# Kernel optimization log

Hardware: AMD Instinct MI355X
Metric: run time of the kernel (lower is better)

## Reference

```python
import jax, jax.numpy as jnp
import numpy as np

N = 100000   # nodes
E = 1600000  # edges (avg degree 16)
D = 128      # in_channels == hidden_channels
H = 4        # heads
C = D // H   # per-head channels = 32


def leaky(x, slope):
    return jnp.where(x >= 0, x, slope * x)


def setup_inputs() -> dict:
    key = jax.random.key(0)
    ks = jax.random.split(key, 12)
    s = 1.0 / np.sqrt(D)
    return {
        "x": jax.random.normal(ks[0], (N, D), jnp.float32),
        "edge_index": jax.random.randint(ks[1], (2, E), 0, N, jnp.int32),
        "edge_type": jax.random.randint(ks[2], (E,), 0, 8, jnp.int32),
        # linear1 (first_layer=True): LeakyReLU(0.01) -> Linear(D, D)
        "W1": jax.random.normal(ks[3], (D, D), jnp.float32) * s,
        "b1": jnp.zeros((D,), jnp.float32),
        # GATConv params: lin (no bias), att_src/att_dst [1,H,C], output bias [H*C]
        "Wg": jax.random.normal(ks[4], (D, D), jnp.float32) * s,
        "att_src": jax.random.normal(ks[5], (1, H, C), jnp.float32) * s,
        "att_dst": jax.random.normal(ks[6], (1, H, C), jnp.float32) * s,
        "bias_g": jnp.zeros((D,), jnp.float32),
        # linear2: LeakyReLU(0.01) -> Linear(D, D)
        "W2": jax.random.normal(ks[7], (D, D), jnp.float32) * s,
        "b2": jnp.zeros((D,), jnp.float32),
    }


def reference(x, edge_index, edge_type, W1, b1, Wg, att_src, att_dst, bias_g, W2, b2):
    # dropout layers act in eval mode (identity); edge_type is unused by forward.
    # linear1: LeakyReLU(0.01) then Linear
    x = leaky(x, 0.01) @ W1.T + b1                      # [N, D]

    # GATConv (add_self_loops=False, concat heads)
    h = (x @ Wg.T).reshape(N, H, C)                     # [N, H, C]
    a_src = jnp.sum(h * att_src, axis=-1)               # [N, H]
    a_dst = jnp.sum(h * att_dst, axis=-1)               # [N, H]

    src, dst = edge_index[0], edge_index[1]
    alpha = leaky(a_src[src] + a_dst[dst], 0.2)          # [E, H]

    # segment softmax over destination nodes (numerically stable)
    amax = jax.ops.segment_max(alpha, dst, num_segments=N)   # [N, H], -inf for empty
    amax = jnp.where(jnp.isfinite(amax), amax, 0.0)
    ex = jnp.exp(alpha - amax[dst])                      # [E, H]
    denom = jax.ops.segment_sum(ex, dst, num_segments=N) # [N, H]
    coeff = ex / (denom[dst] + 1e-16)                    # [E, H]

    msg = h[src] * coeff[:, :, None]                     # [E, H, C]
    out = jax.ops.segment_sum(msg, dst, num_segments=N)  # [N, H, C]
    out = out.reshape(N, H * C) + bias_g                 # [N, D]

    # linear2: LeakyReLU(0.01) then Linear; Dropout(0.3) identity at eval
    out = leaky(out, 0.01) @ W2.T + b2                   # [N, D]
    return out
```

## Files before the change

kernel.cpp:

```cpp
#include <hip/hip_runtime.h>
#include <hip/hip_bf16.h>

#define D128 128

typedef __attribute__((ext_vector_type(8))) short bf16x8;
typedef __attribute__((ext_vector_type(4))) float f32x4;

__device__ __forceinline__ float b2f(unsigned short u) {
    union { unsigned int i; float f; } z;
    z.i = ((unsigned int)u) << 16;
    return z.f;
}

__device__ __forceinline__ unsigned short f2b(float f) {
    union { float f; unsigned int i; } z;
    z.f = f;
    unsigned int r = z.i + 0x7FFFu + ((z.i >> 16) & 1u);
    return (unsigned short)(r >> 16);
}

__device__ __forceinline__ f32x4 mfma16(bf16x8 a, bf16x8 b, f32x4 c) {
    return __builtin_amdgcn_mfma_f32_16x16x32_bf16(a, b, c, 0, 0, 0);
}

#define CHUNK 8192
#define MAXBINS 512
#define BINCAP 8192
#define XBB 1536

__global__ __launch_bounds__(256) void k_prep1(
    const float* __restrict__ x,
    const float* __restrict__ W1, const float* __restrict__ Wg,
    const float* __restrict__ b1,
    const int* __restrict__ ei, int* __restrict__ M,
    float* __restrict__ Wc, float* __restrict__ bc,
    unsigned short* __restrict__ xb,
    int N, int E, int B, int nbins)
{
    __shared__ float wgr[256];
    __shared__ int hist[MAXBINS];
    const int t = threadIdx.x;
    if (blockIdx.x < 64) {
        const int i0 = blockIdx.x * 2;
        wgr[t] = Wg[i0 * 128 + t];
        __syncthreads();
        const int half = t >> 7;
        const int j = t & 127;
        const float* wr = &wgr[half * 128];
        float acc = 0.f;
        #pragma unroll 4
        for (int k = 0; k < 128; ++k)
            acc += wr[k] * W1[k * 128 + j];
        Wc[(i0 + half) * 128 + j] = acc;
        if (j == 0) {
            float ab = 0.f;
            for (int k = 0; k < 128; ++k) ab += wr[k] * b1[k];
            bc[i0 + half] = ab;
        }
    } else if (blockIdx.x < 64 + B) {
        const int chunk = blockIdx.x - 64;
        for (int i = t; i < nbins; i += 256) hist[i] = 0;
        __syncthreads();
        const int base = chunk * CHUNK;
        const int end = min(base + CHUNK, E);
        for (int e = base + t; e < end; e += 256)
            atomicAdd(&hist[ei[E + e] >> 8], 1);
        __syncthreads();
        for (int i = t; i < nbins; i += 256)
            M[i * B + chunk] = hist[i];
    } else {
        const size_t total = (size_t)N * 128;
        const size_t stride = (size_t)XBB * 256 * 8;
        for (size_t i = ((size_t)(blockIdx.x - 64 - B) * 256 + t) * 8; i + 8 <= total; i += stride) {
            float4 f0 = *(const float4*)(x + i);
            float4 f1 = *(const float4*)(x + i + 4);
            float v[8] = { f0.x, f0.y, f0.z, f0.w, f1.x, f1.y, f1.z, f1.w };
            union { uint4 q; unsigned short s[8]; } o;
            #pragma unroll
            for (int jj = 0; jj < 8; ++jj) {
                float f = v[jj];
                f = f >= 0.f ? f : 0.01f * f;
                o.s[jj] = f2b(f);
            }
            *(uint4*)(xb + i) = o.q;
        }
    }
}

__global__ __launch_bounds__(256) void k_prep2s(
    const float* __restrict__ Wc, const float* __restrict__ bc,
    const float* __restrict__ att_s, const float* __restrict__ att_d,
    const float* __restrict__ W2,
    unsigned short* __restrict__ Wcat, unsigned short* __restrict__ W2l,
    float* __restrict__ lbias,
    const int* __restrict__ M, int* __restrict__ scanned,
    int* __restrict__ bsum, int nM)
{
    __shared__ int lds[256];
    const int b = blockIdx.x, t = threadIdx.x;
    if (b < 9) {
        const int q = b * 256 + t;
        const int ct = q >> 8, rem = q & 255;
        const int ks = rem >> 6, lane = rem & 63;
        const int ldiv = lane >> 4, lmod = lane & 15;
        const int kb = ks * 32 + ldiv * 8;
        float v[8];
        if (ct < 8) {
            const int rho = ct * 16 + lmod;
            const float4 a = *(const float4*)(Wc + rho * 128 + kb);
            const float4 bq = *(const float4*)(Wc + rho * 128 + kb + 4);
            v[0] = a.x; v[1] = a.y; v[2] = a.z; v[3] = a.w;
            v[4] = bq.x; v[5] = bq.y; v[6] = bq.z; v[7] = bq.w;
        } else {
            #pragma unroll
            for (int e = 0; e < 8; ++e) v[e] = 0.f;
            if (lmod < 8) {
                const int hh = lmod & 3;
                const float* av = lmod < 4 ? att_s : att_d;
                for (int c = 0; c < 32; ++c) {
                    const float w = av[hh * 32 + c];
                    const float* wrow = Wc + (hh * 32 + c) * 128 + kb;
                    #pragma unroll
                    for (int e = 0; e < 8; ++e) v[e] += w * wrow[e];
                }
            }
        }
        union { uint4 qq; unsigned short s[8]; } o;
        #pragma unroll
        for (int e = 0; e < 8; ++e) o.s[e] = f2b(v[e]);
        *(uint4*)(Wcat + q * 8) = o.qq;
    } else if (b < 17) {
        const int q = (b - 9) * 256 + t;
        const int ct = q >> 8, rem = q & 255;
        const int ks = rem >> 6, lane = rem & 63;
        const int ldiv = lane >> 4, lmod = lane & 15;
        const int kb = ks * 32 + ldiv * 8;
        const int rho = ct * 16 + lmod;
        const float4 a = *(const float4*)(W2 + rho * 128 + kb);
        const float4 bq = *(const float4*)(W2 + rho * 128 + kb + 4);
        union { uint4 qq; unsigned short s[8]; } o;
        o.s[0] = f2b(a.x); o.s[1] = f2b(a.y); o.s[2] = f2b(a.z); o.s[3] = f2b(a.w);
        o.s[4] = f2b(bq.x); o.s[5] = f2b(bq.y); o.s[6] = f2b(bq.z); o.s[7] = f2b(bq.w);
        *(uint4*)(W2l + q * 8) = o.qq;
    } else if (b == 17) {
        if (t < 144) {
            float v = 0.f;
            if (t < 128) v = bc[t];
            else if (t < 136) {
                const int hh = (t - 128) & 3;
                const float* av = t < 132 ? att_s : att_d;
                for (int c = 0; c < 32; ++c) v += av[hh * 32 + c] * bc[hh * 32 + c];
            }
            lbias[t] = v;
        }
    } else {
        const int sid = b - 18;
        const int g0 = sid * 1024 + t * 4;
        int v0 = g0     < nM ? M[g0]     : 0;
        int v1 = g0 + 1 < nM ? M[g0 + 1] : 0;
        int v2 = g0 + 2 < nM ? M[g0 + 2] : 0;
        int v3 = g0 + 3 < nM ? M[g0 + 3] : 0;
        const int s = v0 + v1 + v2 + v3;
        lds[t] = s;
        __syncthreads();
        #pragma unroll
        for (int off = 1; off < 256; off <<= 1) {
            int tv = t >= off ? lds[t - off] : 0;
            __syncthreads();
            lds[t] += tv;
            __syncthreads();
        }
        int run = lds[t] - s;
        if (g0     < nM) scanned[g0]     = run;
        run += v0;
        if (g0 + 1 < nM) scanned[g0 + 1] = run;
        run += v1;
        if (g0 + 2 < nM) scanned[g0 + 2] = run;
        run += v2;
        if (g0 + 3 < nM) scanned[g0 + 3] = run;
        if (t == 255) bsum[sid] = lds[255];
    }
}

__global__ __launch_bounds__(256) void k_gemmA2(
    const unsigned short* __restrict__ xb,
    const unsigned short* __restrict__ Wcat,
    const float* __restrict__ lbias,
    unsigned short* __restrict__ hfeat,
    float* __restrict__ asrc, float* __restrict__ adst,
    const int* __restrict__ ei, const int* __restrict__ scanned,
    const int* __restrict__ bsum, int2* __restrict__ binned,
    int N, int E, int B, int nbins, int nM, int nbg)
{
    __shared__ __align__(16) unsigned char smem[36864];
    const int t = threadIdx.x;
    if (blockIdx.x < nbg) {
        unsigned short* sW = (unsigned short*)smem;
        const int wave = t >> 6, lane = t & 63, lmod = lane & 15, ldiv = lane >> 4;
        const int rowBase = blockIdx.x * 64;

        uint4 w[9];
        #pragma unroll
        for (int r = 0; r < 9; ++r)
            w[r] = *(const uint4*)(Wcat + r * 2048 + t * 8);

        int row = rowBase + wave * 16 + lmod;
        row = min(row, N - 1);
        bf16x8 afr[4];
        #pragma unroll
        for (int ks = 0; ks < 4; ++ks)
            afr[ks] = *(const bf16x8*)(xb + (size_t)row * D128 + ks * 32 + ldiv * 8);

        #pragma unroll
        for (int r = 0; r < 9; ++r)
            *(uint4*)&sW[r * 2048 + t * 8] = w[r];
        __syncthreads();

        f32x4 acc[9] = {};
        #pragma unroll
        for (int ct = 0; ct < 9; ++ct) {
            #pragma unroll
            for (int ks = 0; ks < 4; ++ks) {
                bf16x8 bfr = *(const bf16x8*)&sW[(ct * 256 + ks * 64 + lane) * 8];
                acc[ct] = mfma16(afr[ks], bfr, acc[ct]);
            }
        }

        const int orow = rowBase + wave * 16 + ldiv * 4;
        #pragma unroll
        for (int ct = 0; ct < 8; ++ct) {
            const int col = ct * 16 + lmod;
            const float bias = lbias[col];
            #pragma unroll
            for (int r = 0; r < 4; ++r)
                if (orow + r < N)
                    hfeat[(size_t)(orow + r) * D128 + col] = f2b(acc[ct][r] + bias);
        }
        if (lmod < 8) {
            const float lb = lbias[128 + lmod];
            float* dst = lmod < 4 ? asrc : adst;
            const int hh = lmod & 3;
            #pragma unroll
            for (int r = 0; r < 4; ++r)
                if (orow + r < N)
                    dst[(size_t)(orow + r) * 4 + hh] = acc[8][r] + lb;
        }
    } else {
        int* cursor = (int*)smem;
        int* bpre   = (int*)(smem + MAXBINS * 4);
        const int chunk = blockIdx.x - nbg;
        const int nsb = (nM + 1023) >> 10;
        for (int i = t; i < nsb; i += 256) bpre[i] = bsum[i];
        __syncthreads();
        if (t == 0) {
            int run = 0;
            for (int i = 0; i < nsb; ++i) { int tv = bpre[i]; bpre[i] = run; run += tv; }
        }
        __syncthreads();
        for (int i = t; i < nbins; i += 256) {
            const int idx = i * B + chunk;
            cursor[i] = scanned[idx] + bpre[idx >> 10];
        }
        __syncthreads();
        const int base = chunk * CHUNK;
        const int end = min(base + CHUNK, E);
        for (int e = base + t; e < end; e += 256) {
            const int s = ei[e], d = ei[E + e];
            const int pos = atomicAdd(&cursor[d >> 8], 1);
            binned[pos] = make_int2(s, d);
        }
    }
}

__global__ __launch_bounds__(256) void kB(
    const int2* __restrict__ binned, const int* __restrict__ scanned,
    const int* __restrict__ bsum, int* __restrict__ bucket,
    int* __restrict__ rowstart, int* __restrict__ rowend,
    int E, int B, int nbins, int N, int nM)
{
    __shared__ int2 eb[BINCAP];
    __shared__ int ldeg[256];
    __shared__ int lscan[256];
    __shared__ int lcur[256];
    __shared__ int bpre[1024];
    const int nsb = (nM + 1023) >> 10;
    for (int i = threadIdx.x; i < nsb; i += 256) bpre[i] = bsum[i];
    __syncthreads();
    if (threadIdx.x == 0) {
        int run = 0;
        for (int i = 0; i < nsb; ++i) { int tv = bpre[i]; bpre[i] = run; run += tv; }
    }
    __syncthreads();
    const int bin = blockIdx.x;
    const int i0 = bin * B;
    const int binstart = scanned[i0] + bpre[i0 >> 10];
    int binend;
    if (bin + 1 < nbins) {
        const int i1 = (bin + 1) * B;
        binend = scanned[i1] + bpre[i1 >> 10];
    } else {
        binend = E;
    }
    int n = binend - binstart;
    if (n > BINCAP) n = BINCAP;

    for (int i = threadIdx.x; i < n; i += 256) eb[i] = binned[binstart + i];
    ldeg[threadIdx.x] = 0;
    __syncthreads();
    for (int i = threadIdx.x; i < n; i += 256)
        atomicAdd(&ldeg[eb[i].y & 255], 1);
    __syncthreads();
    const int v = ldeg[threadIdx.x];
    lscan[threadIdx.x] = v;
    __syncthreads();
    #pragma unroll
    for (int off = 1; off < 256; off <<= 1) {
        int tv = threadIdx.x >= off ? lscan[threadIdx.x - off] : 0;
        __syncthreads();
        lscan[threadIdx.x] += tv;
        __syncthreads();
    }
    const int excl = lscan[threadIdx.x] - v;
    lcur[threadIdx.x] = excl;
    const int d = (bin << 8) + threadIdx.x;
    if (d < N) {
        rowstart[d] = binstart + excl;
        rowend[d]   = binstart + excl + v;
    }
    __syncthreads();
    for (int i = threadIdx.x; i < n; i += 256) {
        const int lp = atomicAdd(&lcur[eb[i].y & 255], 1);
        bucket[binstart + lp] = eb[i].x;
    }
}

__global__ __launch_bounds__(256) void k_gat(
    const int* __restrict__ bucket,
    const int* __restrict__ rowstart, const int* __restrict__ rowend,
    const float* __restrict__ asrc, const float* __restrict__ adst,
    const unsigned short* __restrict__ hfeat,
    const float* __restrict__ bias_g,
    unsigned short* __restrict__ outbf, int N)
{
    const int wave = threadIdx.x >> 6;
    const int lane = threadIdx.x & 63;
    const int g    = lane >> 4;
    const int gl   = lane & 15;
    const int h    = gl >> 2;
    const int d    = blockIdx.x * 16 + wave * 4 + g;

    int start = 0, end = 0;
    float a_d = 0.f;
    if (d < N) {
        start = rowstart[d];
        end   = rowend[d];
        a_d   = adst[(size_t)d * 4 + h];
    }
    const unsigned int chb = (unsigned int)(gl << 3);
    const unsigned short* hbase = hfeat + chb;

    float acc[8] = {0.f, 0.f, 0.f, 0.f, 0.f, 0.f, 0.f, 0.f};
    float denom = 0.f;

    int j = start;
    for (; j + 2 <= end; j += 2) {
        const int s0 = __builtin_nontemporal_load(bucket + j);
        const int s1 = __builtin_nontemporal_load(bucket + j + 1);
        const float as0 = asrc[((size_t)s0 << 2) + h];
        const float as1 = asrc[((size_t)s1 << 2) + h];
        const uint4 hp0 = *(const uint4*)(hbase + ((unsigned int)s0 << 7));
        const uint4 hp1 = *(const uint4*)(hbase + ((unsigned int)s1 << 7));
        float a0 = as0 + a_d; a0 = a0 >= 0.f ? a0 : 0.2f * a0;
        float a1 = as1 + a_d; a1 = a1 >= 0.f ? a1 : 0.2f * a1;
        const float w0 = __expf(a0), w1 = __expf(a1);
        denom += w0 + w1;
        acc[0] += w0 * b2f((unsigned short)(hp0.x & 0xFFFFu)) + w1 * b2f((unsigned short)(hp1.x & 0xFFFFu));
        acc[1] += w0 * b2f((unsigned short)(hp0.x >> 16))     + w1 * b2f((unsigned short)(hp1.x >> 16));
        acc[2] += w0 * b2f((unsigned short)(hp0.y & 0xFFFFu)) + w1 * b2f((unsigned short)(hp1.y & 0xFFFFu));
        acc[3] += w0 * b2f((unsigned short)(hp0.y >> 16))     + w1 * b2f((unsigned short)(hp1.y >> 16));
        acc[4] += w0 * b2f((unsigned short)(hp0.z & 0xFFFFu)) + w1 * b2f((unsigned short)(hp1.z & 0xFFFFu));
        acc[5] += w0 * b2f((unsigned short)(hp0.z >> 16))     + w1 * b2f((unsigned short)(hp1.z >> 16));
        acc[6] += w0 * b2f((unsigned short)(hp0.w & 0xFFFFu)) + w1 * b2f((unsigned short)(hp1.w & 0xFFFFu));
        acc[7] += w0 * b2f((unsigned short)(hp0.w >> 16))     + w1 * b2f((unsigned short)(hp1.w >> 16));
    }
    if (j < end) {
        const int s0 = __builtin_nontemporal_load(bucket + j);
        const float as0 = asrc[((size_t)s0 << 2) + h];
        const uint4 hp0 = *(const uint4*)(hbase + ((unsigned int)s0 << 7));
        float a0 = as0 + a_d; a0 = a0 >= 0.f ? a0 : 0.2f * a0;
        const float w0 = __expf(a0);
        denom += w0;
        acc[0] += w0 * b2f((unsigned short)(hp0.x & 0xFFFFu));
        acc[1] += w0 * b2f((unsigned short)(hp0.x >> 16));
        acc[2] += w0 * b2f((unsigned short)(hp0.y & 0xFFFFu));
        acc[3] += w0 * b2f((unsigned short)(hp0.y >> 16));
        acc[4] += w0 * b2f((unsigned short)(hp0.z & 0xFFFFu));
        acc[5] += w0 * b2f((unsigned short)(hp0.z >> 16));
        acc[6] += w0 * b2f((unsigned short)(hp0.w & 0xFFFFu));
        acc[7] += w0 * b2f((unsigned short)(hp0.w >> 16));
    }

    if (d < N) {
        const float inv = 1.f / (denom + 1e-16f);
        const float4 bg0 = *(const float4*)(bias_g + chb);
        const float4 bg1 = *(const float4*)(bias_g + chb + 4);
        const float bg[8] = { bg0.x, bg0.y, bg0.z, bg0.w, bg1.x, bg1.y, bg1.z, bg1.w };
        unsigned short s[8];
        #pragma unroll
        for (int k2 = 0; k2 < 8; ++k2) {
            float v = acc[k2] * inv + bg[k2];
            v = v >= 0.f ? v : 0.01f * v;
            s[k2] = f2b(v);
        }
        uint4 o;
        o.x = ((unsigned int)s[1] << 16) | s[0];
        o.y = ((unsigned int)s[3] << 16) | s[2];
        o.z = ((unsigned int)s[5] << 16) | s[4];
        o.w = ((unsigned int)s[7] << 16) | s[6];
        *(uint4*)(outbf + (((unsigned int)d << 7) + chb)) = o;
    }
}

__global__ __launch_bounds__(256) void k_final(
    const unsigned short* __restrict__ gatbf,
    const unsigned short* __restrict__ W2l,
    const float* __restrict__ b2,
    float* __restrict__ out, int N)
{
    __shared__ __align__(16) unsigned short sW[16384];
    const int t = threadIdx.x;
    const int wave = t >> 6, lane = t & 63, lmod = lane & 15, ldiv = lane >> 4;
    const int rowBase = blockIdx.x * 64;

    uint4 w[8];
    #pragma unroll
    for (int r = 0; r < 8; ++r)
        w[r] = *(const uint4*)(W2l + r * 2048 + t * 8);

    int row = rowBase + wave * 16 + lmod;
    row = min(row, N - 1);
    bf16x8 afr[4];
    #pragma unroll
    for (int ks = 0; ks < 4; ++ks)
        afr[ks] = *(const bf16x8*)(gatbf + (size_t)row * D128 + ks * 32 + ldiv * 8);

    #pragma unroll
    for (int r = 0; r < 8; ++r)
        *(uint4*)&sW[r * 2048 + t * 8] = w[r];
    __syncthreads();

    f32x4 acc[8] = {};
    #pragma unroll
    for (int ct = 0; ct < 8; ++ct) {
        #pragma unroll
        for (int ks = 0; ks < 4; ++ks) {
            bf16x8 bfr = *(const bf16x8*)&sW[(ct * 256 + ks * 64 + lane) * 8];
            acc[ct] = mfma16(afr[ks], bfr, acc[ct]);
        }
    }

    const int orow = rowBase + wave * 16 + ldiv * 4;
    #pragma unroll
    for (int ct = 0; ct < 8; ++ct) {
        const int col = ct * 16 + lmod;
        const float bb = b2[col];
        #pragma unroll
        for (int r = 0; r < 4; ++r)
            if (orow + r < N)
                out[(size_t)(orow + r) * D128 + col] = acc[ct][r] + bb;
    }
}

extern "C" void kernel_launch(void* const* d_in, const int* in_sizes, int n_in,
                              void* d_out, int out_size, void* d_ws, size_t ws_size,
                              hipStream_t stream)
{
    const float* x    = (const float*)d_in[0];
    const int*   ei   = (const int*)d_in[1];
    const float* W1   = (const float*)d_in[3];
    const float* b1   = (const float*)d_in[4];
    const float* Wg   = (const float*)d_in[5];
    const float* atts = (const float*)d_in[6];
    const float* attd = (const float*)d_in[7];
    const float* bg   = (const float*)d_in[8];
    const float* W2   = (const float*)d_in[9];
    const float* b2   = (const float*)d_in[10];
    float* out = (float*)d_out;

    const int N = in_sizes[0] / D128;
    const int E = in_sizes[1] / 2;

    const int B     = (E + CHUNK - 1) / CHUNK;
    const int nbins = (N + 255) >> 8;
    const int nM    = nbins * B;
    const int nsb   = (nM + 1023) / 1024;

    char* ws = (char*)d_ws;
    float* Wc = (float*)ws;
    size_t off = 65536;
    float* bc    = (float*)(ws + off); off += 512;
    float* lbias = (float*)(ws + off); off += 1024;
    unsigned short* Wcat = (unsigned short*)(ws + off); off += 36864;
    unsigned short* W2l  = (unsigned short*)(ws + off); off += 32768;
    unsigned short* xb   = (unsigned short*)(ws + off); off += (size_t)N * D128 * 2;
    unsigned short* hfeat = (unsigned short*)(ws + off); off += (size_t)N * D128 * 2;
    float* asrc = (float*)(ws + off); off += (size_t)N * 4 * 4;
    float* adst = (float*)(ws + off); off += (size_t)N * 4 * 4;
    int* M       = (int*)(ws + off); off += (size_t)nM * 4;
    int* scanned = (int*)(ws + off); off += (size_t)nM * 4;
    int* bsum    = (int*)(ws + off); off += 1024 * 4;
    int2* binned = (int2*)(ws + off); off += (size_t)E * 8;
    int* bucket  = (int*)(ws + off); off += (size_t)E * 4;
    int* rowstart = (int*)(ws + off); off += (size_t)N * 4;
    int* rowend   = (int*)(ws + off); off += (size_t)N * 4;
    unsigned short* outbf = (unsigned short*)(ws + off); off += (size_t)N * D128 * 2;

    k_prep1<<<64 + B + XBB, 256, 0, stream>>>(x, W1, Wg, b1, ei, M, Wc, bc, xb,
                                              N, E, B, nbins);
    k_prep2s<<<18 + nsb, 256, 0, stream>>>(Wc, bc, atts, attd, W2, Wcat, W2l,
                                           lbias, M, scanned, bsum, nM);
    const int nbg = (N + 63) / 64;
    k_gemmA2<<<nbg + B, 256, 0, stream>>>(xb, Wcat, lbias, hfeat, asrc, adst,
                                          ei, scanned, bsum, binned,
                                          N, E, B, nbins, nM, nbg);
    kB<<<nbins, 256, 0, stream>>>(binned, scanned, bsum, bucket,
                                  rowstart, rowend, E, B, nbins, N, nM);
    k_gat<<<(N + 15) / 16, 256, 0, stream>>>(bucket, rowstart, rowend,
                                             asrc, adst, hfeat, bg, outbf, N);
    k_final<<<nbg, 256, 0, stream>>>(outbf, W2l, b2, out, N);
}
```

Measured before the change: 320.4 us.

## Fuse input bf16 conversion into GEMM, pack binned edges into 32 bits

The separate pass that applied LeakyReLU and converted x to bf16 in k_prep1 is removed. The GEMM kernel now reads fp32 x directly and converts it in registers, which avoids writing and re-reading a bf16 copy of x. Binned edges are packed into one 32-bit word (local dst in the high bits, src in the low 20 bits), halving the traffic and LDS footprint of the binning stage. Nontemporal loads of the bucket array in the GAT kernel become plain loads. The packing assumes N stays below 2^20.

```diff
diff --git a/kernel.cpp b/kernel.cpp
--- a/kernel.cpp
+++ b/kernel.cpp
@@ -26,16 +26,13 @@
 #define CHUNK 8192
 #define MAXBINS 512
 #define BINCAP 8192
-#define XBB 1536
 
 __global__ __launch_bounds__(256) void k_prep1(
-    const float* __restrict__ x,
     const float* __restrict__ W1, const float* __restrict__ Wg,
     const float* __restrict__ b1,
     const int* __restrict__ ei, int* __restrict__ M,
     float* __restrict__ Wc, float* __restrict__ bc,
-    unsigned short* __restrict__ xb,
-    int N, int E, int B, int nbins)
+    int E, int B, int nbins)
 {
     __shared__ float wgr[256];
     __shared__ int hist[MAXBINS];
@@ -57,7 +54,7 @@
             for (int k = 0; k < 128; ++k) ab += wr[k] * b1[k];
             bc[i0 + half] = ab;
         }
-    } else if (blockIdx.x < 64 + B) {
+    } else {
         const int chunk = blockIdx.x - 64;
         for (int i = t; i < nbins; i += 256) hist[i] = 0;
         __syncthreads();
@@ -68,22 +65,6 @@
         __syncthreads();
         for (int i = t; i < nbins; i += 256)
             M[i * B + chunk] = hist[i];
-    } else {
-        const size_t total = (size_t)N * 128;
-        const size_t stride = (size_t)XBB * 256 * 8;
-        for (size_t i = ((size_t)(blockIdx.x - 64 - B) * 256 + t) * 8; i + 8 <= total; i += stride) {
-            float4 f0 = *(const float4*)(x + i);
-            float4 f1 = *(const float4*)(x + i + 4);
-            float v[8] = { f0.x, f0.y, f0.z, f0.w, f1.x, f1.y, f1.z, f1.w };
-            union { uint4 q; unsigned short s[8]; } o;
-            #pragma unroll
-            for (int jj = 0; jj < 8; ++jj) {
-                float f = v[jj];
-                f = f >= 0.f ? f : 0.01f * f;
-                o.s[jj] = f2b(f);
-            }
-            *(uint4*)(xb + i) = o.q;
-        }
     }
 }
 
@@ -183,13 +164,13 @@
 }
 
 __global__ __launch_bounds__(256) void k_gemmA2(
-    const unsigned short* __restrict__ xb,
+    const float* __restrict__ x,
     const unsigned short* __restrict__ Wcat,
     const float* __restrict__ lbias,
     unsigned short* __restrict__ hfeat,
     float* __restrict__ asrc, float* __restrict__ adst,
     const int* __restrict__ ei, const int* __restrict__ scanned,
-    const int* __restrict__ bsum, int2* __restrict__ binned,
+    const int* __restrict__ bsum, unsigned int* __restrict__ binned,
     int N, int E, int B, int nbins, int nM, int nbg)
 {
     __shared__ __align__(16) unsigned char smem[36864];
@@ -208,8 +189,20 @@
         row = min(row, N - 1);
         bf16x8 afr[4];
         #pragma unroll
-        for (int ks = 0; ks < 4; ++ks)
-            afr[ks] = *(const bf16x8*)(xb + (size_t)row * D128 + ks * 32 + ldiv * 8);
+        for (int ks = 0; ks < 4; ++ks) {
+            const float* px = x + (size_t)row * D128 + ks * 32 + ldiv * 8;
+            float4 f0 = *(const float4*)px;
+            float4 f1 = *(const float4*)(px + 4);
+            float tmp[8] = { f0.x, f0.y, f0.z, f0.w, f1.x, f1.y, f1.z, f1.w };
+            union { bf16x8 v; unsigned short s[8]; } o;
+            #pragma unroll
+            for (int jj = 0; jj < 8; ++jj) {
+                float f = tmp[jj];
+                f = f >= 0.f ? f : 0.01f * f;
+                o.s[jj] = f2b(f);
+            }
+            afr[ks] = o.v;
+        }
 
         #pragma unroll
         for (int r = 0; r < 9; ++r)
@@ -267,18 +260,18 @@
         for (int e = base + t; e < end; e += 256) {
             const int s = ei[e], d = ei[E + e];
             const int pos = atomicAdd(&cursor[d >> 8], 1);
-            binned[pos] = make_int2(s, d);
+            binned[pos] = ((unsigned int)(d & 255) << 20) | (unsigned int)s;
         }
     }
 }
 
 __global__ __launch_bounds__(256) void kB(
-    const int2* __restrict__ binned, const int* __restrict__ scanned,
+    const unsigned int* __restrict__ binned, const int* __restrict__ scanned,
     const int* __restrict__ bsum, int* __restrict__ bucket,
     int* __restrict__ rowstart, int* __restrict__ rowend,
     int E, int B, int nbins, int N, int nM)
 {
-    __shared__ int2 eb[BINCAP];
+    __shared__ unsigned int eb[BINCAP];
     __shared__ int ldeg[256];
     __shared__ int lscan[256];
     __shared__ int lcur[256];
@@ -308,7 +301,7 @@
     ldeg[threadIdx.x] = 0;
     __syncthreads();
     for (int i = threadIdx.x; i < n; i += 256)
-        atomicAdd(&ldeg[eb[i].y & 255], 1);
+        atomicAdd(&ldeg[eb[i] >> 20], 1);
     __syncthreads();
     const int v = ldeg[threadIdx.x];
     lscan[threadIdx.x] = v;
@@ -329,8 +322,9 @@
     }
     __syncthreads();
     for (int i = threadIdx.x; i < n; i += 256) {
-        const int lp = atomicAdd(&lcur[eb[i].y & 255], 1);
-        bucket[binstart + lp] = eb[i].x;
+        const unsigned int p = eb[i];
+        const int lp = atomicAdd(&lcur[p >> 20], 1);
+        bucket[binstart + lp] = (int)(p & 0xFFFFFu);
     }
 }
 
@@ -364,8 +358,8 @@
 
     int j = start;
     for (; j + 2 <= end; j += 2) {
-        const int s0 = __builtin_nontemporal_load(bucket + j);
-        const int s1 = __builtin_nontemporal_load(bucket + j + 1);
+        const int s0 = bucket[j];
+        const int s1 = bucket[j + 1];
         const float as0 = asrc[((size_t)s0 << 2) + h];
         const float as1 = asrc[((size_t)s1 << 2) + h];
         const uint4 hp0 = *(const uint4*)(hbase + ((unsigned int)s0 << 7));
@@ -384,7 +378,7 @@
         acc[7] += w0 * b2f((unsigned short)(hp0.w >> 16))     + w1 * b2f((unsigned short)(hp1.w >> 16));
     }
     if (j < end) {
-        const int s0 = __builtin_nontemporal_load(bucket + j);
+        const int s0 = bucket[j];
         const float as0 = asrc[((size_t)s0 << 2) + h];
         const uint4 hp0 = *(const uint4*)(hbase + ((unsigned int)s0 << 7));
         float a0 = as0 + a_d; a0 = a0 >= 0.f ? a0 : 0.2f * a0;
@@ -502,25 +496,23 @@
     float* lbias = (float*)(ws + off); off += 1024;
     unsigned short* Wcat = (unsigned short*)(ws + off); off += 36864;
     unsigned short* W2l  = (unsigned short*)(ws + off); off += 32768;
-    unsigned short* xb   = (unsigned short*)(ws + off); off += (size_t)N * D128 * 2;
     unsigned short* hfeat = (unsigned short*)(ws + off); off += (size_t)N * D128 * 2;
     float* asrc = (float*)(ws + off); off += (size_t)N * 4 * 4;
     float* adst = (float*)(ws + off); off += (size_t)N * 4 * 4;
     int* M       = (int*)(ws + off); off += (size_t)nM * 4;
     int* scanned = (int*)(ws + off); off += (size_t)nM * 4;
     int* bsum    = (int*)(ws + off); off += 1024 * 4;
-    int2* binned = (int2*)(ws + off); off += (size_t)E * 8;
+    unsigned int* binned = (unsigned int*)(ws + off); off += (size_t)E * 4;
     int* bucket  = (int*)(ws + off); off += (size_t)E * 4;
     int* rowstart = (int*)(ws + off); off += (size_t)N * 4;
     int* rowend   = (int*)(ws + off); off += (size_t)N * 4;
     unsigned short* outbf = (unsigned short*)(ws + off); off += (size_t)N * D128 * 2;
 
-    k_prep1<<<64 + B + XBB, 256, 0, stream>>>(x, W1, Wg, b1, ei, M, Wc, bc, xb,
-                                              N, E, B, nbins);
+    k_prep1<<<64 + B, 256, 0, stream>>>(W1, Wg, b1, ei, M, Wc, bc, E, B, nbins);
     k_prep2s<<<18 + nsb, 256, 0, stream>>>(Wc, bc, atts, attd, W2, Wcat, W2l,
                                            lbias, M, scanned, bsum, nM);
     const int nbg = (N + 63) / 64;
-    k_gemmA2<<<nbg + B, 256, 0, stream>>>(xb, Wcat, lbias, hfeat, asrc, adst,
+    k_gemmA2<<<nbg + B, 256, 0, stream>>>(x, Wcat, lbias, hfeat, asrc, adst,
                                           ei, scanned, bsum, binned,
                                           N, E, B, nbins, nM, nbg);
     kB<<<nbins, 256, 0, stream>>>(binned, scanned, bsum, bucket,
```

New measurement: 291.9 us. 8.9% less time.
